# Performance work log

Hardware: AMD Instinct MI355X
Metric: run time of the kernel (lower is better)

The kernel has to match this reference:

```python
import jax, jax.numpy as jnp
import numpy as np

D = 512          # input_dim == hidden size of MinLSTM layers
OUT = 1          # output_dim of fc_out
B, T = 8, 4096
LN_EPS = 1e-5


def _linear_params(key, d_in, d_out):
    kw, kb = jax.random.split(key)
    lim = 1.0 / np.sqrt(d_in)
    W = jax.random.uniform(kw, (d_out, d_in), minval=-lim, maxval=lim, dtype=jnp.float32)
    b = jax.random.uniform(kb, (d_out,), minval=-lim, maxval=lim, dtype=jnp.float32)
    return W, b


def setup_inputs() -> dict:
    key = jax.random.key(0)
    ks = jax.random.split(key, 8)
    x = jax.random.normal(ks[0], (B, T, D), dtype=jnp.float32)
    Wf0, bf0 = _linear_params(ks[1], D, D)
    Wi0, bi0 = _linear_params(ks[2], D, D)
    Wh0, bh0 = _linear_params(ks[3], D, D)
    Wf1, bf1 = _linear_params(ks[4], D, D)
    Wi1, bi1 = _linear_params(ks[5], D, D)
    Wh1, bh1 = _linear_params(ks[6], D, D)
    W_out, b_out = _linear_params(ks[7], D, OUT)
    ln_g = jnp.ones((D,), dtype=jnp.float32)
    ln_b = jnp.zeros((D,), dtype=jnp.float32)
    return {
        'x': x,
        'Wf0': Wf0, 'bf0': bf0, 'Wi0': Wi0, 'bi0': bi0, 'Wh0': Wh0, 'bh0': bh0,
        'Wf1': Wf1, 'bf1': bf1, 'Wi1': Wi1, 'bi1': bi1, 'Wh1': Wh1, 'bh1': bh1,
        'ln_g': ln_g, 'ln_b': ln_b, 'W_out': W_out, 'b_out': b_out,
    }


def _minlstm(x, Wf, bf, Wi, bi, Wh, bh):
    # minLSTM (parallel form, h0 = 0):
    #   f = sigma(W_f x), i = sigma(W_i x), h~ = W_h x
    #   f' = f/(f+i), i' = i/(f+i)
    #   h_t = f'_t * h_{t-1} + i'_t * h~_t   (linear recurrence -> associative scan)
    f = jax.nn.sigmoid(jnp.einsum('btd,ed->bte', x, Wf) + bf)
    i = jax.nn.sigmoid(jnp.einsum('btd,ed->bte', x, Wi) + bi)
    h_tilde = jnp.einsum('btd,ed->bte', x, Wh) + bh
    denom = f + i
    a = f / denom                      # decay coefficient f'
    u = (i / denom) * h_tilde          # input contribution i' * h~

    def combine(c1, c2):
        a1, u1 = c1
        a2, u2 = c2
        return a1 * a2, a2 * u1 + u2

    _, h = jax.lax.associative_scan(combine, (a, u), axis=1)
    return h  # [B, T, D]


def reference(x, Wf0, bf0, Wi0, bi0, Wh0, bh0,
              Wf1, bf1, Wi1, bi1, Wh1, bh1,
              ln_g, ln_b, W_out, b_out):
    h = _minlstm(x, Wf0, bf0, Wi0, bi0, Wh0, bh0)
    h = _minlstm(h, Wf1, bf1, Wi1, bi1, Wh1, bh1)
    h = jnp.where(jnp.isnan(h), x, h)      # NaN fallback to input
    h = x + h                               # residual
    # LayerNorm over last dim
    mu = jnp.mean(h, axis=-1, keepdims=True)
    var = jnp.mean(jnp.square(h - mu), axis=-1, keepdims=True)
    hn = (h - mu) * jax.lax.rsqrt(var + LN_EPS) * ln_g + ln_b
    # output projection [B, T, OUT]
    return jnp.einsum('btd,od->bto', hn, W_out) + b_out
```

## Files before the change

kernel.cpp:

```cpp
#include <hip/hip_runtime.h>
#include <hip/hip_bf16.h>
#include <stdint.h>


#define MROWS 32768
#define DDIM  512
#define TLEN  4096
#define BSZ   8
#define NCHUNK 64
#define CLEN   64

typedef __attribute__((ext_vector_type(8))) __bf16 bf16x8;
typedef __attribute__((ext_vector_type(4))) float f32x4;
typedef __attribute__((ext_vector_type(4))) unsigned short ushort4_t;
typedef __attribute__((ext_vector_type(2))) unsigned short ushort2_t;

static __device__ __forceinline__ unsigned short f2bf(float f) {
    unsigned int u = __float_as_uint(f);
    u = (u + 0x7FFFu + ((u >> 16) & 1u)) >> 16;
    return (unsigned short)u;
}
static __device__ __forceinline__ float bf2f(unsigned short s) {
    return __uint_as_float(((unsigned int)s) << 16);
}
static __device__ __forceinline__ void gload_lds16(const void* gptr, void* ldsp) {
    __builtin_amdgcn_global_load_lds(
        (const __attribute__((address_space(1))) uint32_t*)gptr,
        (__attribute__((address_space(3))) uint32_t*)ldsp,
        16, 0, 0);
}

#define WAITV(n) asm volatile("s_waitcnt vmcnt(" #n ")" ::: "memory")

__global__ __launch_bounds__(256) void cast_all(
    const float4* __restrict__ x,
    const float4* __restrict__ w0, const float4* __restrict__ w1,
    const float4* __restrict__ w2, const float4* __restrict__ w3,
    const float4* __restrict__ w4, const float4* __restrict__ w5,
    ushort4_t* __restrict__ xb, ushort4_t* __restrict__ wb)
{
    int i = blockIdx.x * 256 + threadIdx.x;
    float4 v;
    ushort4_t* dst;
    if (i < 4194304) {
        v = x[i];
        dst = xb + i;
    } else {
        int j = i - 4194304;
        int wsel = j >> 16;
        int rem = j & 65535;
        const float4* src = (wsel == 0) ? w0 : (wsel == 1) ? w1 : (wsel == 2) ? w2
                          : (wsel == 3) ? w3 : (wsel == 4) ? w4 : w5;
        v = src[rem];
        dst = wb + j;
    }
    ushort4_t o;
    o.x = f2bf(v.x); o.y = f2bf(v.y); o.z = f2bf(v.z); o.w = f2bf(v.w);
    *dst = o;
}

__global__ __launch_bounds__(512, 2) void gates_gemm(
    const unsigned short* __restrict__ X,
    const unsigned short* __restrict__ Wf,
    const unsigned short* __restrict__ Wi,
    const unsigned short* __restrict__ Wh,
    const float* __restrict__ bf_, const float* __restrict__ bi_,
    const float* __restrict__ bh_,
    unsigned int* __restrict__ au_out)
{
    __shared__ __align__(16) unsigned short lds[2 * 16384];

    const int tid  = threadIdx.x;
    const int lane = tid & 63;
    const int wave = tid >> 6;
    const int wm = wave >> 2, wn = wave & 3;
    const int lr  = lane & 15;
    const int kgl = lane >> 4;

    const int w = blockIdx.x;
    const int xcd = w & 7;
    const int s = w >> 3;
    const int by = xcd * 32 + (s >> 2);
    const int bx = s & 3;
    const int mblk = by * 128;
    const int nblk = bx * 128;

    const int srow = tid >> 2;
    const int sg   = ((tid & 3) ^ ((srow >> 1) & 3)) << 3;
    const int tid8 = tid * 8;
    const unsigned short* pA = X  + (size_t)(mblk + srow) * 512 + sg;
    const unsigned short* pF = Wf + (size_t)(nblk + srow) * 512 + sg;
    const unsigned short* pI = Wi + (size_t)(nblk + srow) * 512 + sg;
    const unsigned short* pH = Wh + (size_t)(nblk + srow) * 512 + sg;

    int aoff[4], boff[2];
#pragma unroll
    for (int mi = 0; mi < 4; ++mi) {
        int row = wm * 64 + mi * 16 + lr;
        aoff[mi] = row * 32 + (((kgl ^ (row >> 1)) & 3) << 3);
    }
#pragma unroll
    for (int ni = 0; ni < 2; ++ni) {
        int row = wn * 32 + ni * 16 + lr;
        boff[ni] = row * 32 + (((kgl ^ (row >> 1)) & 3) << 3);
    }

    f32x4 accF[4][2], accI[4][2], accH[4][2];
    const f32x4 zero = {0.f, 0.f, 0.f, 0.f};
#pragma unroll
    for (int mi = 0; mi < 4; ++mi)
#pragma unroll
        for (int ni = 0; ni < 2; ++ni) {
            accF[mi][ni] = zero; accI[mi][ni] = zero; accH[mi][ni] = zero;
        }

#define STAGE(bufp) do { \
    gload_lds16(pA, (bufp) + tid8);          \
    gload_lds16(pF, (bufp) + 4096 + tid8);   \
    gload_lds16(pI, (bufp) + 8192 + tid8);   \
    gload_lds16(pH, (bufp) + 12288 + tid8);  \
    pA += 32; pF += 32; pI += 32; pH += 32; } while (0)

    STAGE(lds);

#pragma unroll
    for (int t = 0; t < 16; ++t) {
        if (t < 15) {
            STAGE(lds + ((t + 1) & 1) * 16384);
            WAITV(4);
        } else {
            WAITV(0);
        }
        __builtin_amdgcn_s_barrier();
        __builtin_amdgcn_sched_barrier(0);

        const unsigned short* cb = lds + (t & 1) * 16384;
        bf16x8 af[4];
#pragma unroll
        for (int mi = 0; mi < 4; ++mi)
            af[mi] = *reinterpret_cast<const bf16x8*>(cb + aoff[mi]);
        bf16x8 bF[2], bI[2], bH[2];
#pragma unroll
        for (int ni = 0; ni < 2; ++ni) {
            bF[ni] = *reinterpret_cast<const bf16x8*>(cb + 4096  + boff[ni]);
            bI[ni] = *reinterpret_cast<const bf16x8*>(cb + 8192  + boff[ni]);
            bH[ni] = *reinterpret_cast<const bf16x8*>(cb + 12288 + boff[ni]);
        }
        __builtin_amdgcn_s_setprio(1);
#pragma unroll
        for (int mi = 0; mi < 4; ++mi)
#pragma unroll
            for (int ni = 0; ni < 2; ++ni) {
                accF[mi][ni] = __builtin_amdgcn_mfma_f32_16x16x32_bf16(af[mi], bF[ni], accF[mi][ni], 0, 0, 0);
                accI[mi][ni] = __builtin_amdgcn_mfma_f32_16x16x32_bf16(af[mi], bI[ni], accI[mi][ni], 0, 0, 0);
                accH[mi][ni] = __builtin_amdgcn_mfma_f32_16x16x32_bf16(af[mi], bH[ni], accH[mi][ni], 0, 0, 0);
            }
        __builtin_amdgcn_s_setprio(0);
        __builtin_amdgcn_sched_barrier(0);
        __builtin_amdgcn_s_barrier();
        __builtin_amdgcn_sched_barrier(0);
    }
#undef STAGE

#pragma unroll
    for (int ni = 0; ni < 2; ++ni) {
        const int n = nblk + wn * 32 + ni * 16 + lr;
        const float bfv = bf_[n], biv = bi_[n], bhv = bh_[n];
#pragma unroll
        for (int mi = 0; mi < 4; ++mi) {
#pragma unroll
            for (int r = 0; r < 4; ++r) {
                const int m = mblk + wm * 64 + mi * 16 + kgl * 4 + r;
                float zf = accF[mi][ni][r] + bfv;
                float zi = accI[mi][ni][r] + biv;
                float zh = accH[mi][ni][r] + bhv;
                float ef = __expf(-zf);
                float ei = __expf(-zi);
                float inv = __frcp_rn(2.0f + ef + ei);
                float av = (1.0f + ei) * inv;
                float uv = (1.0f + ef) * inv * zh;
                au_out[(size_t)m * 512 + n] =
                    ((unsigned int)f2bf(uv) << 16) | (unsigned int)f2bf(av);
            }
        }
    }
}

__global__ void scan_pass1(const uint4* __restrict__ au,
                           float4* __restrict__ Asum, float4* __restrict__ Usum) {
    int gid = blockIdx.x * 256 + threadIdx.x;
    int d4 = gid & 127;
    int c  = (gid >> 7) & 63;
    int b  = gid >> 13;
    size_t base = (size_t)(b * TLEN + c * CLEN) * 128 + d4;
    float A[4] = {1.f, 1.f, 1.f, 1.f};
    float h[4] = {0.f, 0.f, 0.f, 0.f};
#pragma unroll 4
    for (int l = 0; l < CLEN; ++l) {
        uint4 v = au[base + (size_t)l * 128];
        unsigned int vv[4] = {v.x, v.y, v.z, v.w};
#pragma unroll
        for (int j = 0; j < 4; ++j) {
            float av = __uint_as_float(vv[j] << 16);
            float uv = __uint_as_float(vv[j] & 0xFFFF0000u);
            A[j] *= av;
            h[j] = av * h[j] + uv;
        }
    }
    size_t s4 = (size_t)(b * NCHUNK + c) * 128 + d4;
    Asum[s4] = make_float4(A[0], A[1], A[2], A[3]);
    Usum[s4] = make_float4(h[0], h[1], h[2], h[3]);
}

__global__ void scan_pass2(const float4* __restrict__ Asum, const float4* __restrict__ Usum,
                           float4* __restrict__ Hinit) {
    int t = blockIdx.x * 256 + threadIdx.x;
    int d4 = t & 127;
    int b = t >> 7;
    float4 h = {0.f, 0.f, 0.f, 0.f};
    for (int c = 0; c < NCHUNK; ++c) {
        size_t idx = (size_t)(b * NCHUNK + c) * 128 + d4;
        Hinit[idx] = h;
        float4 A = Asum[idx]; float4 U = Usum[idx];
        h.x = A.x * h.x + U.x; h.y = A.y * h.y + U.y;
        h.z = A.z * h.z + U.z; h.w = A.w * h.w + U.w;
    }
}

__global__ void scan_pass3(const uint4* __restrict__ au,
                           const float4* __restrict__ Hinit,
                           ushort4_t* __restrict__ hout) {
    int gid = blockIdx.x * 256 + threadIdx.x;
    int d4 = gid & 127;
    int c  = (gid >> 7) & 63;
    int b  = gid >> 13;
    size_t base = (size_t)(b * TLEN + c * CLEN) * 128 + d4;
    size_t s4 = (size_t)(b * NCHUNK + c) * 128 + d4;
    float4 h0 = Hinit[s4];
    float h[4] = {h0.x, h0.y, h0.z, h0.w};
#pragma unroll 4
    for (int l = 0; l < CLEN; ++l) {
        size_t idx = base + (size_t)l * 128;
        uint4 v = au[idx];
        unsigned int vv[4] = {v.x, v.y, v.z, v.w};
        ushort4_t o;
#pragma unroll
        for (int j = 0; j < 4; ++j) {
            float av = __uint_as_float(vv[j] << 16);
            float uv = __uint_as_float(vv[j] & 0xFFFF0000u);
            h[j] = av * h[j] + uv;
            o[j] = f2bf(h[j]);
        }
        hout[idx] = o;
    }
}

__global__ __launch_bounds__(256) void final_kernel(
    const float* __restrict__ x, const unsigned short* __restrict__ h1,
    const float* __restrict__ g, const float* __restrict__ bvec,
    const float* __restrict__ Wout, const float* __restrict__ bout,
    float* __restrict__ out)
{
    int row = blockIdx.x;
    int tid = threadIdx.x;
    size_t base = (size_t)row * 512;
    ushort2_t hv2 = *reinterpret_cast<const ushort2_t*>(h1 + base + tid * 2);
    float2 xv2 = *reinterpret_cast<const float2*>(x + base + tid * 2);
    float r[2];
#pragma unroll
    for (int j = 0; j < 2; ++j) {
        float hv = bf2f(hv2[j]);
        float xv = (j == 0) ? xv2.x : xv2.y;
        if (hv != hv) hv = xv;
        r[j] = xv + hv;
    }
    float s = r[0] + r[1];
    float q = r[0] * r[0] + r[1] * r[1];
#pragma unroll
    for (int m = 32; m >= 1; m >>= 1) {
        s += __shfl_xor(s, m);
        q += __shfl_xor(q, m);
    }
    __shared__ float ss[4], sq[4], sp[4];
    int w = tid >> 6, lane = tid & 63;
    if (lane == 0) { ss[w] = s; sq[w] = q; }
    __syncthreads();
    float tot  = ss[0] + ss[1] + ss[2] + ss[3];
    float totq = sq[0] + sq[1] + sq[2] + sq[3];
    float mu = tot * (1.0f / 512.0f);
    float var = totq * (1.0f / 512.0f) - mu * mu;
    float rstd = rsqrtf(var + 1e-5f);
    float p = 0.0f;
#pragma unroll
    for (int j = 0; j < 2; ++j) {
        int d = tid * 2 + j;
        float nv = (r[j] - mu) * rstd * g[d] + bvec[d];
        p += nv * Wout[d];
    }
#pragma unroll
    for (int m = 32; m >= 1; m >>= 1) p += __shfl_xor(p, m);
    if (lane == 0) sp[w] = p;
    __syncthreads();
    if (tid == 0) out[row] = sp[0] + sp[1] + sp[2] + sp[3] + bout[0];
}

extern "C" void kernel_launch(void* const* d_in, const int* in_sizes, int n_in,
                              void* d_out, int out_size, void* d_ws, size_t ws_size,
                              hipStream_t stream) {
    const float* x    = (const float*)d_in[0];
    const float* Wf0  = (const float*)d_in[1];  const float* bf0 = (const float*)d_in[2];
    const float* Wi0  = (const float*)d_in[3];  const float* bi0 = (const float*)d_in[4];
    const float* Wh0  = (const float*)d_in[5];  const float* bh0 = (const float*)d_in[6];
    const float* Wf1  = (const float*)d_in[7];  const float* bf1 = (const float*)d_in[8];
    const float* Wi1  = (const float*)d_in[9];  const float* bi1 = (const float*)d_in[10];
    const float* Wh1  = (const float*)d_in[11]; const float* bh1 = (const float*)d_in[12];
    const float* ln_g = (const float*)d_in[13]; const float* ln_b = (const float*)d_in[14];
    const float* W_out = (const float*)d_in[15]; const float* b_out = (const float*)d_in[16];

    char* ws = (char*)d_ws;
    unsigned short* Xb = (unsigned short*)ws;  ws += (size_t)MROWS * DDIM * 2;
    unsigned short* Wball = (unsigned short*)ws;
    unsigned short* Wb[6];
    for (int i = 0; i < 6; ++i) { Wb[i] = (unsigned short*)ws; ws += (size_t)DDIM * DDIM * 2; }
    unsigned int* aubuf = (unsigned int*)ws; ws += (size_t)MROWS * DDIM * 4;
    float* Asum = (float*)ws;  ws += (size_t)BSZ * NCHUNK * DDIM * 4;
    float* Usum = (float*)ws;  ws += (size_t)BSZ * NCHUNK * DDIM * 4;
    float* Hinit = (float*)ws; ws += (size_t)BSZ * NCHUNK * DDIM * 4;
    unsigned short* h0b = (unsigned short*)ws; ws += (size_t)MROWS * DDIM * 2;
    unsigned short* h1b = (unsigned short*)ws; ws += (size_t)MROWS * DDIM * 2;

    cast_all<<<17920, 256, 0, stream>>>(
        (const float4*)x, (const float4*)Wf0, (const float4*)Wi0, (const float4*)Wh0,
        (const float4*)Wf1, (const float4*)Wi1, (const float4*)Wh1,
        (ushort4_t*)Xb, (ushort4_t*)Wball);

    gates_gemm<<<1024, 512, 0, stream>>>(Xb, Wb[0], Wb[1], Wb[2], bf0, bi0, bh0, aubuf);
    scan_pass1<<<256, 256, 0, stream>>>((const uint4*)aubuf, (float4*)Asum, (float4*)Usum);
    scan_pass2<<<4, 256, 0, stream>>>((const float4*)Asum, (const float4*)Usum, (float4*)Hinit);
    scan_pass3<<<256, 256, 0, stream>>>((const uint4*)aubuf, (const float4*)Hinit, (ushort4_t*)h0b);

    gates_gemm<<<1024, 512, 0, stream>>>(h0b, Wb[3], Wb[4], Wb[5], bf1, bi1, bh1, aubuf);
    scan_pass1<<<256, 256, 0, stream>>>((const uint4*)aubuf, (float4*)Asum, (float4*)Usum);
    scan_pass2<<<4, 256, 0, stream>>>((const float4*)Asum, (const float4*)Usum, (float4*)Hinit);
    scan_pass3<<<256, 256, 0, stream>>>((const uint4*)aubuf, (const float4*)Hinit, (ushort4_t*)h1b);

    final_kernel<<<MROWS, 256, 0, stream>>>(x, h1b, ln_g, ln_b, W_out, b_out, (float*)d_out);
}
```

Baseline: 257.1 us.

## Fuse chunk scan into GEMM epilogue and scan-pass3 with LayerNorm output

```diff
diff --git a/kernel.cpp b/kernel.cpp
--- a/kernel.cpp
+++ b/kernel.cpp
@@ -13,7 +13,6 @@
 typedef __attribute__((ext_vector_type(8))) __bf16 bf16x8;
 typedef __attribute__((ext_vector_type(4))) float f32x4;
 typedef __attribute__((ext_vector_type(4))) unsigned short ushort4_t;
-typedef __attribute__((ext_vector_type(2))) unsigned short ushort2_t;
 
 static __device__ __forceinline__ unsigned short f2bf(float f) {
     unsigned int u = __float_as_uint(f);
@@ -59,96 +58,116 @@
     *dst = o;
 }
 
-__global__ __launch_bounds__(512, 2) void gates_gemm(
+__global__ __launch_bounds__(512, 4) void gates_gemm(
     const unsigned short* __restrict__ X,
     const unsigned short* __restrict__ Wf,
     const unsigned short* __restrict__ Wi,
     const unsigned short* __restrict__ Wh,
     const float* __restrict__ bf_, const float* __restrict__ bi_,
     const float* __restrict__ bh_,
-    unsigned int* __restrict__ au_out)
+    unsigned int* __restrict__ au_out,
+    float* __restrict__ Asum, float* __restrict__ Usum)
 {
-    __shared__ __align__(16) unsigned short lds[2 * 16384];
+    __shared__ __align__(16) unsigned short lds[2 * 10240];
 
     const int tid  = threadIdx.x;
     const int lane = tid & 63;
     const int wave = tid >> 6;
-    const int wm = wave >> 2, wn = wave & 3;
+    const int wm = wave >> 1;
+    const int wn = wave & 1;
     const int lr  = lane & 15;
     const int kgl = lane >> 4;
 
     const int w = blockIdx.x;
     const int xcd = w & 7;
     const int s = w >> 3;
-    const int by = xcd * 32 + (s >> 2);
-    const int bx = s & 3;
+    const int by = xcd * 32 + (s >> 3);
+    const int bx = s & 7;
     const int mblk = by * 128;
-    const int nblk = bx * 128;
-
-    const int srow = tid >> 2;
-    const int sg   = ((tid & 3) ^ ((srow >> 1) & 3)) << 3;
-    const int tid8 = tid * 8;
-    const unsigned short* pA = X  + (size_t)(mblk + srow) * 512 + sg;
-    const unsigned short* pF = Wf + (size_t)(nblk + srow) * 512 + sg;
-    const unsigned short* pI = Wi + (size_t)(nblk + srow) * 512 + sg;
-    const unsigned short* pH = Wh + (size_t)(nblk + srow) * 512 + sg;
-
-    int aoff[4], boff[2];
-#pragma unroll
-    for (int mi = 0; mi < 4; ++mi) {
-        int row = wm * 64 + mi * 16 + lr;
+    const int nblk = bx * 64;
+
+    const int r4 = lane >> 2;
+    const int c4 = lane & 3;
+    const unsigned short *g0, *g1, *g2;
+    int o0, o1, o2;
+    {
+        const int sb = (wave < 4) ? wave * 3 : 12 + (wave - 4) * 2;
+        const int sl2 = (wave < 4) ? sb + 2 : sb + 1;
+        const int sls[3] = {sb, sb + 1, sl2};
+        const unsigned short* gp[3];
+        int of[3];
+#pragma unroll
+        for (int i = 0; i < 3; ++i) {
+            int sl = sls[i];
+            const unsigned short* src;
+            int lrow, grow;
+            if (sl < 8)       { src = X;  lrow = sl * 16 + r4;        grow = mblk + lrow; }
+            else if (sl < 12) { src = Wf; lrow = (sl - 8) * 16 + r4;  grow = nblk + lrow; }
+            else if (sl < 16) { src = Wi; lrow = (sl - 12) * 16 + r4; grow = nblk + lrow; }
+            else              { src = Wh; lrow = (sl - 16) * 16 + r4; grow = nblk + lrow; }
+            int cg = ((c4 ^ (lrow >> 1)) & 3) << 3;
+            gp[i] = src + (size_t)grow * 512 + cg;
+            of[i] = sl * 512 + r4 * 32 + c4 * 8;
+        }
+        g0 = gp[0]; g1 = gp[1]; g2 = gp[2];
+        o0 = of[0]; o1 = of[1]; o2 = of[2];
+    }
+
+    int aoff[2], boff[2];
+#pragma unroll
+    for (int mi = 0; mi < 2; ++mi) {
+        int row = wm * 32 + mi * 16 + lr;
         aoff[mi] = row * 32 + (((kgl ^ (row >> 1)) & 3) << 3);
     }
 #pragma unroll
     for (int ni = 0; ni < 2; ++ni) {
         int row = wn * 32 + ni * 16 + lr;
-        boff[ni] = row * 32 + (((kgl ^ (row >> 1)) & 3) << 3);
-    }
-
-    f32x4 accF[4][2], accI[4][2], accH[4][2];
+        boff[ni] = 4096 + row * 32 + (((kgl ^ (row >> 1)) & 3) << 3);
+    }
+
+    f32x4 accF[2][2], accI[2][2], accH[2][2];
     const f32x4 zero = {0.f, 0.f, 0.f, 0.f};
 #pragma unroll
-    for (int mi = 0; mi < 4; ++mi)
+    for (int mi = 0; mi < 2; ++mi)
 #pragma unroll
         for (int ni = 0; ni < 2; ++ni) {
             accF[mi][ni] = zero; accI[mi][ni] = zero; accH[mi][ni] = zero;
         }
 
-#define STAGE(bufp) do { \
-    gload_lds16(pA, (bufp) + tid8);          \
-    gload_lds16(pF, (bufp) + 4096 + tid8);   \
-    gload_lds16(pI, (bufp) + 8192 + tid8);   \
-    gload_lds16(pH, (bufp) + 12288 + tid8);  \
-    pA += 32; pF += 32; pI += 32; pH += 32; } while (0)
-
-    STAGE(lds);
+#define STAGE(bb) do { \
+    gload_lds16(g0, lds + (bb) + o0); \
+    gload_lds16(g1, lds + (bb) + o1); \
+    if (wave < 4) gload_lds16(g2, lds + (bb) + o2); \
+    g0 += 32; g1 += 32; g2 += 32; } while (0)
+
+    STAGE(0);
 
 #pragma unroll
     for (int t = 0; t < 16; ++t) {
         if (t < 15) {
-            STAGE(lds + ((t + 1) & 1) * 16384);
-            WAITV(4);
+            STAGE(((t + 1) & 1) * 10240);
+            if (wave < 4) { WAITV(3); } else { WAITV(2); }
         } else {
             WAITV(0);
         }
         __builtin_amdgcn_s_barrier();
         __builtin_amdgcn_sched_barrier(0);
 
-        const unsigned short* cb = lds + (t & 1) * 16384;
-        bf16x8 af[4];
-#pragma unroll
-        for (int mi = 0; mi < 4; ++mi)
+        const unsigned short* cb = lds + (t & 1) * 10240;
+        bf16x8 af[2];
+#pragma unroll
+        for (int mi = 0; mi < 2; ++mi)
             af[mi] = *reinterpret_cast<const bf16x8*>(cb + aoff[mi]);
         bf16x8 bF[2], bI[2], bH[2];
 #pragma unroll
         for (int ni = 0; ni < 2; ++ni) {
-            bF[ni] = *reinterpret_cast<const bf16x8*>(cb + 4096  + boff[ni]);
-            bI[ni] = *reinterpret_cast<const bf16x8*>(cb + 8192  + boff[ni]);
-            bH[ni] = *reinterpret_cast<const bf16x8*>(cb + 12288 + boff[ni]);
+            bF[ni] = *reinterpret_cast<const bf16x8*>(cb + boff[ni]);
+            bI[ni] = *reinterpret_cast<const bf16x8*>(cb + 2048 + boff[ni]);
+            bH[ni] = *reinterpret_cast<const bf16x8*>(cb + 4096 + boff[ni]);
         }
         __builtin_amdgcn_s_setprio(1);
 #pragma unroll
-        for (int mi = 0; mi < 4; ++mi)
+        for (int mi = 0; mi < 2; ++mi)
 #pragma unroll
             for (int ni = 0; ni < 2; ++ni) {
                 accF[mi][ni] = __builtin_amdgcn_mfma_f32_16x16x32_bf16(af[mi], bF[ni], accF[mi][ni], 0, 0, 0);
@@ -162,15 +181,18 @@
     }
 #undef STAGE
 
+    float pa[2], pu[2];
 #pragma unroll
     for (int ni = 0; ni < 2; ++ni) {
         const int n = nblk + wn * 32 + ni * 16 + lr;
         const float bfv = bf_[n], biv = bi_[n], bhv = bh_[n];
-#pragma unroll
-        for (int mi = 0; mi < 4; ++mi) {
+        float ca = 1.f, cu = 0.f;
+#pragma unroll
+        for (int mi = 0; mi < 2; ++mi) {
+            float sa = 1.f, su = 0.f;
 #pragma unroll
             for (int r = 0; r < 4; ++r) {
-                const int m = mblk + wm * 64 + mi * 16 + kgl * 4 + r;
+                const int m = mblk + wm * 32 + mi * 16 + kgl * 4 + r;
                 float zf = accF[mi][ni][r] + bfv;
                 float zi = accI[mi][ni][r] + biv;
                 float zh = accH[mi][ni][r] + bhv;
@@ -181,35 +203,40 @@
                 float uv = (1.0f + ef) * inv * zh;
                 au_out[(size_t)m * 512 + n] =
                     ((unsigned int)f2bf(uv) << 16) | (unsigned int)f2bf(av);
+                sa *= av; su = av * su + uv;
             }
-        }
-    }
-}
-
-__global__ void scan_pass1(const uint4* __restrict__ au,
-                           float4* __restrict__ Asum, float4* __restrict__ Usum) {
-    int gid = blockIdx.x * 256 + threadIdx.x;
-    int d4 = gid & 127;
-    int c  = (gid >> 7) & 63;
-    int b  = gid >> 13;
-    size_t base = (size_t)(b * TLEN + c * CLEN) * 128 + d4;
-    float A[4] = {1.f, 1.f, 1.f, 1.f};
-    float h[4] = {0.f, 0.f, 0.f, 0.f};
-#pragma unroll 4
-    for (int l = 0; l < CLEN; ++l) {
-        uint4 v = au[base + (size_t)l * 128];
-        unsigned int vv[4] = {v.x, v.y, v.z, v.w};
-#pragma unroll
-        for (int j = 0; j < 4; ++j) {
-            float av = __uint_as_float(vv[j] << 16);
-            float uv = __uint_as_float(vv[j] & 0xFFFF0000u);
-            A[j] *= av;
-            h[j] = av * h[j] + uv;
-        }
-    }
-    size_t s4 = (size_t)(b * NCHUNK + c) * 128 + d4;
-    Asum[s4] = make_float4(A[0], A[1], A[2], A[3]);
-    Usum[s4] = make_float4(h[0], h[1], h[2], h[3]);
+            float oa = __shfl_xor(sa, 16), ou = __shfl_xor(su, 16);
+            bool up = (lane & 16) != 0;
+            float ta = sa * oa;
+            float tu = up ? (sa * ou + su) : (oa * su + ou);
+            sa = ta; su = tu;
+            oa = __shfl_xor(sa, 32); ou = __shfl_xor(su, 32);
+            up = (lane & 32) != 0;
+            ta = sa * oa;
+            tu = up ? (sa * ou + su) : (oa * su + ou);
+            sa = ta; su = tu;
+            cu = sa * cu + su; ca = ca * sa;
+        }
+        pa[ni] = ca; pu[ni] = cu;
+    }
+    float* sm = (float*)lds;
+    if (kgl == 0) {
+#pragma unroll
+        for (int ni = 0; ni < 2; ++ni) {
+            int nl = wn * 32 + ni * 16 + lr;
+            sm[wm * 64 + nl] = pa[ni];
+            sm[256 + wm * 64 + nl] = pu[ni];
+        }
+    }
+    __syncthreads();
+    if (tid < 128) {
+        int cl = tid >> 6, nl = tid & 63;
+        float a1 = sm[(2 * cl) * 64 + nl],     u1 = sm[256 + (2 * cl) * 64 + nl];
+        float a2 = sm[(2 * cl + 1) * 64 + nl], u2 = sm[256 + (2 * cl + 1) * 64 + nl];
+        size_t ci = (size_t)(by * 2 + cl) * 512 + nblk + nl;
+        Asum[ci] = a1 * a2;
+        Usum[ci] = a2 * u1 + u2;
+    }
 }
 
 __global__ void scan_pass2(const float4* __restrict__ Asum, const float4* __restrict__ Usum,
@@ -255,53 +282,74 @@
     }
 }
 
-__global__ __launch_bounds__(256) void final_kernel(
-    const float* __restrict__ x, const unsigned short* __restrict__ h1,
+__global__ __launch_bounds__(128) void scan3_final(
+    const uint4* __restrict__ au, const float4* __restrict__ Hinit,
+    const float4* __restrict__ x4,
     const float* __restrict__ g, const float* __restrict__ bvec,
     const float* __restrict__ Wout, const float* __restrict__ bout,
     float* __restrict__ out)
 {
-    int row = blockIdx.x;
-    int tid = threadIdx.x;
-    size_t base = (size_t)row * 512;
-    ushort2_t hv2 = *reinterpret_cast<const ushort2_t*>(h1 + base + tid * 2);
-    float2 xv2 = *reinterpret_cast<const float2*>(x + base + tid * 2);
-    float r[2];
-#pragma unroll
-    for (int j = 0; j < 2; ++j) {
-        float hv = bf2f(hv2[j]);
-        float xv = (j == 0) ? xv2.x : xv2.y;
-        if (hv != hv) hv = xv;
-        r[j] = xv + hv;
-    }
-    float s = r[0] + r[1];
-    float q = r[0] * r[0] + r[1] * r[1];
-#pragma unroll
-    for (int m = 32; m >= 1; m >>= 1) {
-        s += __shfl_xor(s, m);
-        q += __shfl_xor(q, m);
-    }
-    __shared__ float ss[4], sq[4], sp[4];
-    int w = tid >> 6, lane = tid & 63;
-    if (lane == 0) { ss[w] = s; sq[w] = q; }
-    __syncthreads();
-    float tot  = ss[0] + ss[1] + ss[2] + ss[3];
-    float totq = sq[0] + sq[1] + sq[2] + sq[3];
-    float mu = tot * (1.0f / 512.0f);
-    float var = totq * (1.0f / 512.0f) - mu * mu;
-    float rstd = rsqrtf(var + 1e-5f);
-    float p = 0.0f;
-#pragma unroll
-    for (int j = 0; j < 2; ++j) {
-        int d = tid * 2 + j;
-        float nv = (r[j] - mu) * rstd * g[d] + bvec[d];
-        p += nv * Wout[d];
-    }
-#pragma unroll
-    for (int m = 32; m >= 1; m >>= 1) p += __shfl_xor(p, m);
-    if (lane == 0) sp[w] = p;
-    __syncthreads();
-    if (tid == 0) out[row] = sp[0] + sp[1] + sp[2] + sp[3] + bout[0];
+    const int blk = blockIdx.x;
+    const int b = blk >> 6, c = blk & 63;
+    const int d4 = threadIdx.x;
+    const int lane = threadIdx.x & 63;
+    const int wv = threadIdx.x >> 6;
+
+    float4 h0 = Hinit[(size_t)blk * 128 + d4];
+    float h[4] = {h0.x, h0.y, h0.z, h0.w};
+    float4 g4 = reinterpret_cast<const float4*>(g)[d4];
+    float4 b4 = reinterpret_cast<const float4*>(bvec)[d4];
+    float4 w4 = reinterpret_cast<const float4*>(Wout)[d4];
+    const float ga[4] = {g4.x, g4.y, g4.z, g4.w};
+    const float ba[4] = {b4.x, b4.y, b4.z, b4.w};
+    const float wa[4] = {w4.x, w4.y, w4.z, w4.w};
+    const float bo = bout[0];
+
+    __shared__ float redS[2], redQ[2], redP[2];
+    size_t base = ((size_t)b * TLEN + c * CLEN) * 128 + d4;
+
+    for (int l = 0; l < CLEN; ++l) {
+        size_t idx = base + (size_t)l * 128;
+        uint4 v = au[idx];
+        float4 xr = x4[idx];
+        const unsigned int vv[4] = {v.x, v.y, v.z, v.w};
+        const float xa[4] = {xr.x, xr.y, xr.z, xr.w};
+        float r[4];
+        float sfl = 0.f, q = 0.f;
+#pragma unroll
+        for (int j = 0; j < 4; ++j) {
+            float av = __uint_as_float(vv[j] << 16);
+            float uv = __uint_as_float(vv[j] & 0xFFFF0000u);
+            h[j] = av * h[j] + uv;
+            float hv = h[j];
+            if (hv != hv) hv = xa[j];
+            float rr = xa[j] + hv;
+            r[j] = rr;
+            sfl += rr; q += rr * rr;
+        }
+#pragma unroll
+        for (int m = 32; m >= 1; m >>= 1) {
+            sfl += __shfl_xor(sfl, m);
+            q += __shfl_xor(q, m);
+        }
+        if (lane == 0) { redS[wv] = sfl; redQ[wv] = q; }
+        __syncthreads();
+        float st = redS[0] + redS[1];
+        float qt = redQ[0] + redQ[1];
+        float mu = st * (1.0f / 512.0f);
+        float var = qt * (1.0f / 512.0f) - mu * mu;
+        float rstd = rsqrtf(var + 1e-5f);
+        float p = 0.f;
+#pragma unroll
+        for (int j = 0; j < 4; ++j)
+            p += ((r[j] - mu) * rstd * ga[j] + ba[j]) * wa[j];
+#pragma unroll
+        for (int m = 32; m >= 1; m >>= 1) p += __shfl_xor(p, m);
+        if (lane == 0) redP[wv] = p;
+        __syncthreads();
+        if (threadIdx.x == 0)
+            out[(size_t)b * TLEN + c * CLEN + l] = redP[0] + redP[1] + bo;
+    }
 }
 
 extern "C" void kernel_launch(void* const* d_in, const int* in_sizes, int n_in,
@@ -327,22 +375,21 @@
     float* Usum = (float*)ws;  ws += (size_t)BSZ * NCHUNK * DDIM * 4;
     float* Hinit = (float*)ws; ws += (size_t)BSZ * NCHUNK * DDIM * 4;
     unsigned short* h0b = (unsigned short*)ws; ws += (size_t)MROWS * DDIM * 2;
-    unsigned short* h1b = (unsigned short*)ws; ws += (size_t)MROWS * DDIM * 2;
 
     cast_all<<<17920, 256, 0, stream>>>(
         (const float4*)x, (const float4*)Wf0, (const float4*)Wi0, (const float4*)Wh0,
         (const float4*)Wf1, (const float4*)Wi1, (const float4*)Wh1,
         (ushort4_t*)Xb, (ushort4_t*)Wball);
 
-    gates_gemm<<<1024, 512, 0, stream>>>(Xb, Wb[0], Wb[1], Wb[2], bf0, bi0, bh0, aubuf);
-    scan_pass1<<<256, 256, 0, stream>>>((const uint4*)aubuf, (float4*)Asum, (float4*)Usum);
+    gates_gemm<<<2048, 512, 0, stream>>>(Xb, Wb[0], Wb[1], Wb[2], bf0, bi0, bh0,
+                                         aubuf, Asum, Usum);
     scan_pass2<<<4, 256, 0, stream>>>((const float4*)Asum, (const float4*)Usum, (float4*)Hinit);
     scan_pass3<<<256, 256, 0, stream>>>((const uint4*)aubuf, (const float4*)Hinit, (ushort4_t*)h0b);
 
-    gates_gemm<<<1024, 512, 0, stream>>>(h0b, Wb[3], Wb[4], Wb[5], bf1, bi1, bh1, aubuf);
-    scan_pass1<<<256, 256, 0, stream>>>((const uint4*)aubuf, (float4*)Asum, (float4*)Usum);
+    gates_gemm<<<2048, 512, 0, stream>>>(h0b, Wb[3], Wb[4], Wb[5], bf1, bi1, bh1,
+                                         aubuf, Asum, Usum);
     scan_pass2<<<4, 256, 0, stream>>>((const float4*)Asum, (const float4*)Usum, (float4*)Hinit);
-    scan_pass3<<<256, 256, 0, stream>>>((const uint4*)aubuf, (const float4*)Hinit, (ushort4_t*)h1b);
-
-    final_kernel<<<MROWS, 256, 0, stream>>>(x, h1b, ln_g, ln_b, W_out, b_out, (float*)d_out);
-}
+    scan3_final<<<512, 128, 0, stream>>>((const uint4*)aubuf, (const float4*)Hinit,
+                                         (const float4*)x, ln_g, ln_b, W_out, b_out,
+                                         (float*)d_out);
+}
```

Result: faster. 246.5 us (-4.1%).
